# Optimization experiments

Hardware: AMD Instinct MI355X
Metric: run time of the kernel (lower is better)

The kernel has to match this reference:

```python
import jax, jax.numpy as jnp
import numpy as np

NU, NI, E = 20000, 8000, 64
DV, DT = 4096, 768
NE, B = 200000, 4096
L_HET, L_HOMO = 2, 1
K_ISG, K_UCG = 10, 20
MMW, WD = 0.1, 1e-4


def setup_inputs() -> dict:
    ks = jax.random.split(jax.random.key(0), 14)
    return {
        "feat_v": jax.random.normal(ks[0], (NI, DV), jnp.float32),
        "feat_t": jax.random.normal(ks[1], (NI, DT), jnp.float32),
        "pref_v": jax.random.normal(ks[2], (NU, E), jnp.float32) * 0.1,
        "pref_t": jax.random.normal(ks[3], (NU, E), jnp.float32) * 0.1,
        "W_v": jax.random.normal(ks[4], (DV, E), jnp.float32) * 0.02,
        "W_t": jax.random.normal(ks[5], (DT, E), jnp.float32) * 0.02,
        "user_v_alpha": jax.random.normal(ks[6], (1,), jnp.float32),
        "user_nb_weights": jax.random.normal(ks[7], (NU, K_UCG), jnp.float32),
        "edge_users": jax.random.randint(ks[8], (NE,), 0, NU, jnp.int32),
        "edge_items": jax.random.randint(ks[9], (NE,), 0, NI, jnp.int32),
        "u_ids": jax.random.randint(ks[10], (B,), 0, NU, jnp.int32),
        "pos_ids": jax.random.randint(ks[11], (B,), 0, NI, jnp.int32),
        "neg_ids": jax.random.randint(ks[12], (B,), 0, NI, jnp.int32),
        "user_nb": jax.random.randint(ks[13], (NU, K_UCG), 0, NU, jnp.int32),
    }


def reference(feat_v, feat_t, pref_v, pref_t, W_v, W_t, user_v_alpha,
              user_nb_weights, edge_users, edge_items, u_ids, pos_ids,
              neg_ids, user_nb):
    N = NU + NI
    # bidirectional bipartite edges (items offset by NU)
    src = jnp.concatenate([edge_users, edge_items + NU])
    dst = jnp.concatenate([edge_items + NU, edge_users])
    deg = jax.ops.segment_sum(jnp.ones_like(src, jnp.float32), dst, num_segments=N)
    deg = jnp.maximum(deg, 1.0)
    norm = (1.0 / jnp.sqrt(deg[src] * deg[dst]))[:, None]

    def hetero_gcn(feat, pref, W):
        x = jnp.concatenate([pref, feat @ W], axis=0)  # [N, E]
        h, out = x, x
        for _ in range(L_HET):
            h = jax.ops.segment_sum(h[src] * norm, dst, num_segments=N)
            out = out + h
        return out[:NU], out[NU:]

    u_v, i_v = hetero_gcn(feat_v, pref_v, W_v)
    u_t, i_t = hetero_gcn(feat_t, pref_t, W_t)
    a_v = jax.nn.sigmoid(user_v_alpha[0])
    u_f = jnp.concatenate([a_v * u_v, (1.0 - a_v) * u_t], axis=1)  # [NU, 2E]
    i_f = jnp.concatenate([i_v, i_t], axis=1)                      # [NI, 2E]

    # Item Semantic Graph: KNN over cosine sim, no grad through adjacency.
    def knn_adj(f):
        fn = f / jnp.linalg.norm(f, axis=-1, keepdims=True)
        sim = fn @ fn.T                       # [NI, NI]
        _, idx = jax.lax.top_k(sim, K_ISG)
        return jnp.zeros((NI, NI), f.dtype).at[jnp.arange(NI)[:, None], idx].set(1.0)

    adj = jax.lax.stop_gradient(MMW * knn_adj(feat_v) + (1.0 - MMW) * knn_adj(feat_t))
    rs = adj.sum(axis=1)
    adj = adj * jnp.where(rs > 0, 1.0 / rs, 0.0)[:, None]

    h_i = i_f
    for _ in range(L_HOMO):
        h_i = adj @ h_i

    # User Co-occurrence Graph: scatter-softmax attention aggregation, vectorized.
    attn = jax.nn.softmax(user_nb_weights, axis=1)  # [NU, K]
    h_u = u_f
    for _ in range(L_HOMO):
        h_u = jnp.einsum('uk,ukd->ud', attn, h_u[user_nb])

    z_u = u_f + h_u
    z_i = i_f + h_i
    pos = jnp.sum(z_u[u_ids] * z_i[pos_ids], axis=1)
    neg = jnp.sum(z_u[u_ids] * z_i[neg_ids], axis=1)
    bpr = -jnp.mean(jax.nn.log_sigmoid(pos - neg))
    reg = WD * (jnp.sum(pref_v ** 2) + jnp.sum(pref_t ** 2) + user_v_alpha[0] ** 2) / 2.0
    return bpr + reg
```

## Files before the change

kernel.cpp:

```cpp
#include <hip/hip_runtime.h>
#include <cstdint>
#include <cstddef>

#define NU_C   20000
#define NI_C   8000
#define NTOT_C 28000
#define NE_C   200000
#define B_C    4096
#define NPAD_C 8064
#define NCHUNK 63
#define NPAIR  2016

typedef unsigned short u16;
typedef unsigned int   u32;
typedef unsigned char  u8;
typedef __bf16 bf16x8 __attribute__((ext_vector_type(8)));
typedef float  f32x4  __attribute__((ext_vector_type(4)));

static __device__ __forceinline__ u16 f2bf(float f) {
  u32 u = __float_as_uint(f);
  return (u16)((u + 0x7fffu + ((u >> 16) & 1u)) >> 16);
}

static __device__ __forceinline__ void gl_lds16(const void* g, void* l) {
  __builtin_amdgcn_global_load_lds(
      (const __attribute__((address_space(1))) void*)g,
      (__attribute__((address_space(3))) void*)l, 16, 0, 0);
}

static __device__ __forceinline__ int xcd_swz(int b) {
  return (b & 7) * (NPAIR / 8) + (b >> 3);
}

__global__ void conv_kernel2(const float* __restrict__ Fv, const float* __restrict__ Ft,
                             u16* __restrict__ Fbv, u16* __restrict__ Fbt,
                             u8* __restrict__ Fv8,
                             float* __restrict__ rnv, float* __restrict__ rnt) {
  int b = blockIdx.x;
  const int tid = threadIdx.x;
  float ss = 0.f;
  if (b < NPAD_C) {
    const int row = b;
    u16* dst  = Fbv + (size_t)row * 4096;
    u8*  dst8 = Fv8 + (size_t)row * 4096;
    if (row < NI_C) {
      const float* src = Fv + (size_t)row * 4096;
      for (int c = tid * 4; c < 4096; c += 1024) {
        float4 f = *(const float4*)(src + c);
        ss += f.x*f.x + f.y*f.y + f.z*f.z + f.w*f.w;
        ushort4 v; v.x = f2bf(f.x); v.y = f2bf(f.y); v.z = f2bf(f.z); v.w = f2bf(f.w);
        *(ushort4*)(dst + c) = v;
        int w8 = __builtin_amdgcn_cvt_pk_fp8_f32(f.x, f.y, 0, false);
        w8 = __builtin_amdgcn_cvt_pk_fp8_f32(f.z, f.w, w8, true);
        *(u32*)(dst8 + c) = (u32)w8;
      }
    } else {
      for (int c = tid * 4; c < 4096; c += 1024) {
        ushort4 v; v.x = v.y = v.z = v.w = 0;
        *(ushort4*)(dst + c) = v;
        *(u32*)(dst8 + c) = 0u;
      }
    }
    #pragma unroll
    for (int off = 32; off; off >>= 1) ss += __shfl_xor(ss, off);
    __shared__ float red[4];
    if ((tid & 63) == 0) red[tid >> 6] = ss;
    __syncthreads();
    if (tid == 0) {
      float s = red[0] + red[1] + red[2] + red[3];
      rnv[row] = (row < NI_C) ? rsqrtf(s) : 0.f;
    }
  } else {
    const int row = b - NPAD_C;
    u16* dst = Fbt + (size_t)row * 768;
    if (row < NI_C) {
      const float* src = Ft + (size_t)row * 768;
      for (int c = tid * 4; c < 768; c += 1024) {
        float4 f = *(const float4*)(src + c);
        ss += f.x*f.x + f.y*f.y + f.z*f.z + f.w*f.w;
        ushort4 v; v.x = f2bf(f.x); v.y = f2bf(f.y); v.z = f2bf(f.z); v.w = f2bf(f.w);
        *(ushort4*)(dst + c) = v;
      }
    } else {
      for (int c = tid * 4; c < 768; c += 1024) {
        ushort4 v; v.x = v.y = v.z = v.w = 0;
        *(ushort4*)(dst + c) = v;
      }
    }
    #pragma unroll
    for (int off = 32; off; off >>= 1) ss += __shfl_xor(ss, off);
    __shared__ float red[4];
    if ((tid & 63) == 0) red[tid >> 6] = ss;
    __syncthreads();
    if (tid == 0) {
      float s = red[0] + red[1] + red[2] + red[3];
      rnt[row] = (row < NI_C) ? rsqrtf(s) : 0.f;
    }
  }
}

__launch_bounds__(256)
__global__ void simtopk_sym_fp8_kernel(const u8* __restrict__ F, const float* __restrict__ rn,
                                       u32* __restrict__ tv) {
  __shared__ __align__(16) char smem[34816];
  u8*    sB   = (u8*)smem;
  u8*    sA   = (u8*)(smem + 16384);
  float* T    = (float*)smem;
  int*   mk   = (int*)smem;
  int*   mk2  = (int*)(smem + 20480);
  float* sRNI = (float*)(smem + 33792);
  float* sRNJ = (float*)(smem + 34304);

  const int tid  = threadIdx.x;
  const int lane = tid & 63;
  const int wv   = tid >> 6;
  const int n15  = lane & 15;
  const int quad = lane >> 4;

  int I = 0, rem = xcd_swz(blockIdx.x);
  { int rowlen = NCHUNK;
    while (rem >= rowlen) { rem -= rowlen; rowlen--; I++; } }
  const int J = I + rem;

  const int l2   = lane >> 2;
  const int lseg = (lane & 3) ^ (l2 & 3) ^ (lane >> 4);
  const u8* gB[2]; const u8* gA[2]; u8* lB[2]; u8* lA[2];
  #pragma unroll
  for (int rep = 0; rep < 2; ++rep) {
    int row = wv * 32 + rep * 16 + l2;
    gB[rep] = F + (size_t)(I * 128 + row) * 4096 + lseg * 16;
    gA[rep] = F + (size_t)(J * 128 + row) * 4096 + lseg * 16;
    lB[rep] = sB + (wv * 32 + rep * 16) * 64;
    lA[rep] = sA + (wv * 32 + rep * 16) * 64;
  }
  const int s_n = (n15 & 3) ^ (n15 >> 2);
  const int q2  = quad >> 1;
  const int q8  = (quad & 1) * 8;
  const int rB0 = (wv * 32 + n15) * 64;
  const int rB1 = rB0 + 16 * 64;

  f32x4 acc[2][8];
  #pragma unroll
  for (int tf = 0; tf < 2; ++tf)
    #pragma unroll
    for (int af = 0; af < 8; ++af) { f32x4 z = {0.f,0.f,0.f,0.f}; acc[tf][af] = z; }

  for (int k0 = 0; k0 < 4096; k0 += 128) {
    __syncthreads();
    gl_lds16(gB[0] + k0,      lB[0]);
    gl_lds16(gB[0] + k0 + 64, lB[0] + 8192);
    gl_lds16(gB[1] + k0,      lB[1]);
    gl_lds16(gB[1] + k0 + 64, lB[1] + 8192);
    gl_lds16(gA[0] + k0,      lA[0]);
    gl_lds16(gA[0] + k0 + 64, lA[0] + 8192);
    gl_lds16(gA[1] + k0,      lA[1]);
    gl_lds16(gA[1] + k0 + 64, lA[1] + 8192);
    if (k0 == 0) {
      if (tid < 128) sRNJ[tid] = rn[J * 128 + tid];
      else           sRNI[tid - 128] = rn[I * 128 + (tid - 128)];
    }
    __syncthreads();
    #pragma unroll
    for (int ksub = 0; ksub < 2; ++ksub) {
      const u8* bBase = sB + ksub * 8192;
      const u8* aBase = sA + ksub * 8192;
      #pragma unroll
      for (int ks = 0; ks < 2; ++ks) {
        const int sw = (((ks * 2 + q2) ^ s_n) << 4) + q8;
        long long b0 = *(const long long*)(bBase + rB0 + sw);
        long long b1 = *(const long long*)(bBase + rB1 + sw);
        #pragma unroll
        for (int af = 0; af < 8; ++af) {
          long long a = *(const long long*)(aBase + (af * 16 + n15) * 64 + sw);
          acc[0][af] = __builtin_amdgcn_mfma_f32_16x16x32_fp8_fp8(a, b0, acc[0][af], 0, 0, 0);
          acc[1][af] = __builtin_amdgcn_mfma_f32_16x16x32_fp8_fp8(a, b1, acc[1][af], 0, 0, 0);
        }
      }
    }
  }

  int bk[2][10];
  #pragma unroll
  for (int tf = 0; tf < 2; ++tf)
    #pragma unroll
    for (int j = 0; j < 10; ++j) bk[tf][j] = 0;

  #pragma unroll
  for (int af = 0; af < 8; ++af) {
    const float4 rn4 = *(const float4*)(sRNJ + af * 16 + quad * 4);
    const float rna[4] = {rn4.x, rn4.y, rn4.z, rn4.w};
    #pragma unroll
    for (int r = 0; r < 4; ++r) {
      const int ci = J * 128 + af * 16 + quad * 4 + r;
      #pragma unroll
      for (int tf = 0; tf < 2; ++tf) {
        float v = acc[tf][af][r] * rna[r];
        int key = (int)((__float_as_uint(v) & 0xFFFFE000u) | (u32)ci);
        if (ci < NI_C && key > bk[tf][9]) {
          bk[tf][9] = key;
          #pragma unroll
          for (int j = 9; j > 0; --j)
            if (bk[tf][j] > bk[tf][j-1]) { int t = bk[tf][j]; bk[tf][j] = bk[tf][j-1]; bk[tf][j-1] = t; }
        }
      }
    }
  }
  __syncthreads();
  #pragma unroll
  for (int tf = 0; tf < 2; ++tf) {
    int rl = wv * 32 + tf * 16 + n15;
    #pragma unroll
    for (int j = 0; j < 10; ++j) mk[rl * 40 + quad * 10 + j] = bk[tf][j];
  }
  __syncthreads();
  if (tid < 128) {
    int* m = mk + tid * 40;
    int h0 = 0, h1 = 10, h2 = 20, h3 = 30;
    int v0 = m[0], v1 = m[10], v2 = m[20], v3 = m[30];
    #pragma unroll
    for (int s = 0; s < 10; ++s) {
      int m01 = v0 > v1 ? v0 : v1, m23 = v2 > v3 ? v2 : v3;
      int mx = m01 > m23 ? m01 : m23;
      mk2[tid * 10 + s] = mx;
      if      (mx == v0) { ++h0; v0 = (h0 < 10) ? m[h0] : (int)0x80000000; }
      else if (mx == v1) { ++h1; v1 = (h1 < 20) ? m[h1] : (int)0x80000000; }
      else if (mx == v2) { ++h2; v2 = (h2 < 30) ? m[h2] : (int)0x80000000; }
      else               { ++h3; v3 = (h3 < 40) ? m[h3] : (int)0x80000000; }
    }
  }
  __syncthreads();
  { u32* o = tv + ((size_t)J * NPAD_C + I * 128) * 10;
    for (int g = tid; g < 1280; g += 256) o[g] = (u32)mk2[g]; }

  if (I == J) return;

  int bj[2][10];
  #pragma unroll
  for (int s = 0; s < 2; ++s)
    #pragma unroll
    for (int j = 0; j < 10; ++j) bj[s][j] = 0;

  #pragma unroll
  for (int tf = 0; tf < 2; ++tf) {
    __syncthreads();
    #pragma unroll
    for (int af = 0; af < 8; ++af)
      #pragma unroll
      for (int r = 0; r < 4; ++r)
        T[(af * 16 + quad * 4 + r) * 66 + wv * 16 + n15] = acc[tf][af][r];
    __syncthreads();
    #pragma unroll
    for (int s = 0; s < 2; ++s) {
      const int c_own = wv * 32 + s * 16 + n15;
      #pragma unroll
      for (int j = 0; j < 16; ++j) {
        const int t  = quad * 32 + tf * 16 + j;
        const int t64 = quad * 16 + j;
        float v = T[c_own * 66 + t64] * sRNI[t];
        const int ti = I * 128 + t;
        int key = (int)((__float_as_uint(v) & 0xFFFFE000u) | (u32)ti);
        if (ti < NI_C && key > bj[s][9]) {
          bj[s][9] = key;
          #pragma unroll
          for (int q = 9; q > 0; --q)
            if (bj[s][q] > bj[s][q-1]) { int tt = bj[s][q]; bj[s][q] = bj[s][q-1]; bj[s][q-1] = tt; }
        }
      }
    }
  }
  __syncthreads();
  #pragma unroll
  for (int s = 0; s < 2; ++s) {
    int rl = wv * 32 + s * 16 + n15;
    #pragma unroll
    for (int j = 0; j < 10; ++j) mk[rl * 40 + quad * 10 + j] = bj[s][j];
  }
  __syncthreads();
  if (tid < 128) {
    int* m = mk + tid * 40;
    int h0 = 0, h1 = 10, h2 = 20, h3 = 30;
    int v0 = m[0], v1 = m[10], v2 = m[20], v3 = m[30];
    #pragma unroll
    for (int s = 0; s < 10; ++s) {
      int m01 = v0 > v1 ? v0 : v1, m23 = v2 > v3 ? v2 : v3;
      int mx = m01 > m23 ? m01 : m23;
      mk2[tid * 10 + s] = mx;
      if      (mx == v0) { ++h0; v0 = (h0 < 10) ? m[h0] : (int)0x80000000; }
      else if (mx == v1) { ++h1; v1 = (h1 < 20) ? m[h1] : (int)0x80000000; }
      else if (mx == v2) { ++h2; v2 = (h2 < 30) ? m[h2] : (int)0x80000000; }
      else               { ++h3; v3 = (h3 < 40) ? m[h3] : (int)0x80000000; }
    }
  }
  __syncthreads();
  { u32* o = tv + ((size_t)I * NPAD_C + J * 128) * 10;
    for (int g = tid; g < 1280; g += 256) o[g] = (u32)mk2[g]; }
}

template<int D>
__launch_bounds__(256)
__global__ void simtopk_sym_kernel(const u16* __restrict__ F, const float* __restrict__ rn,
                                   u32* __restrict__ tv) {
  __shared__ __align__(16) char smem[40960];
  u16*   sB   = (u16*)smem;
  u16*   sA   = (u16*)(smem + 16384);
  float* T    = (float*)smem;
  int*   mk   = (int*)smem;
  int*   mk2  = (int*)(smem + 20480);
  float* sRNI = (float*)(smem + 34816);
  float* sRNJ = (float*)(smem + 35328);

  const int tid  = threadIdx.x;
  const int lane = tid & 63;
  const int wv   = tid >> 6;
  const int n15  = lane & 15;
  const int quad = lane >> 4;

  int I = 0, rem = xcd_swz(blockIdx.x);
  { int rowlen = NCHUNK;
    while (rem >= rowlen) { rem -= rowlen; rowlen--; I++; } }
  const int J = I + rem;

  const int l8  = lane >> 3;
  const int sgu = ((lane & 7) ^ l8) << 3;
  const u16* gB[4]; const u16* gA[4]; u16* lB[4]; u16* lA[4];
  #pragma unroll
  for (int rep = 0; rep < 4; ++rep) {
    int row = wv * 32 + rep * 8 + l8;
    gB[rep] = F + (size_t)(I * 128 + row) * D + sgu;
    gA[rep] = F + (size_t)(J * 128 + row) * D + sgu;
    lB[rep] = sB + wv * 2048 + rep * 512;
    lA[rep] = sA + wv * 2048 + rep * 512;
  }
  const int swu0 = ((quad    ) ^ (n15 & 7)) << 3;
  const int swu1 = ((quad + 4) ^ (n15 & 7)) << 3;
  const int rowB0 = (wv * 32 + n15) * 64;
  const int rowB1 = rowB0 + 16 * 64;

  f32x4 acc[2][8];
  #pragma unroll
  for (int tf = 0; tf < 2; ++tf)
    #pragma unroll
    for (int af = 0; af < 8; ++af) { f32x4 z = {0.f,0.f,0.f,0.f}; acc[tf][af] = z; }

  for (int k0 = 0; k0 < D; k0 += 64) {
    __syncthreads();
    #pragma unroll
    for (int rep = 0; rep < 4; ++rep) gl_lds16(gB[rep] + k0, lB[rep]);
    #pragma unroll
    for (int rep = 0; rep < 4; ++rep) gl_lds16(gA[rep] + k0, lA[rep]);
    if (k0 == 0) {
      if (tid < 128) sRNJ[tid] = rn[J * 128 + tid];
      else           sRNI[tid - 128] = rn[I * 128 + (tid - 128)];
    }
    __syncthreads();
    #pragma unroll
    for (int ks = 0; ks < 2; ++ks) {
      const int swu = ks ? swu1 : swu0;
      bf16x8 b0 = *(const bf16x8*)(sB + rowB0 + swu);
      bf16x8 b1 = *(const bf16x8*)(sB + rowB1 + swu);
      #pragma unroll
      for (int af = 0; af < 8; ++af) {
        bf16x8 a = *(const bf16x8*)(sA + (af * 16 + n15) * 64 + swu);
        acc[0][af] = __builtin_amdgcn_mfma_f32_16x16x32_bf16(a, b0, acc[0][af], 0, 0, 0);
        acc[1][af] = __builtin_amdgcn_mfma_f32_16x16x32_bf16(a, b1, acc[1][af], 0, 0, 0);
      }
    }
  }

  int bk[2][10];
  #pragma unroll
  for (int tf = 0; tf < 2; ++tf)
    #pragma unroll
    for (int j = 0; j < 10; ++j) bk[tf][j] = 0;

  #pragma unroll
  for (int af = 0; af < 8; ++af) {
    const float4 rn4 = *(const float4*)(sRNJ + af * 16 + quad * 4);
    const float rna[4] = {rn4.x, rn4.y, rn4.z, rn4.w};
    #pragma unroll
    for (int r = 0; r < 4; ++r) {
      const int ci = J * 128 + af * 16 + quad * 4 + r;
      #pragma unroll
      for (int tf = 0; tf < 2; ++tf) {
        float v = acc[tf][af][r] * rna[r];
        int key = (int)((__float_as_uint(v) & 0xFFFFE000u) | (u32)ci);
        if (ci < NI_C && key > bk[tf][9]) {
          bk[tf][9] = key;
          #pragma unroll
          for (int j = 9; j > 0; --j)
            if (bk[tf][j] > bk[tf][j-1]) { int t = bk[tf][j]; bk[tf][j] = bk[tf][j-1]; bk[tf][j-1] = t; }
        }
      }
    }
  }
  __syncthreads();
  #pragma unroll
  for (int tf = 0; tf < 2; ++tf) {
    int rl = wv * 32 + tf * 16 + n15;
    #pragma unroll
    for (int j = 0; j < 10; ++j) mk[rl * 40 + quad * 10 + j] = bk[tf][j];
  }
  __syncthreads();
  if (tid < 128) {
    int* m = mk + tid * 40;
    int h0 = 0, h1 = 10, h2 = 20, h3 = 30;
    int v0 = m[0], v1 = m[10], v2 = m[20], v3 = m[30];
    #pragma unroll
    for (int s = 0; s < 10; ++s) {
      int m01 = v0 > v1 ? v0 : v1, m23 = v2 > v3 ? v2 : v3;
      int mx = m01 > m23 ? m01 : m23;
      mk2[tid * 10 + s] = mx;
      if      (mx == v0) { ++h0; v0 = (h0 < 10) ? m[h0] : (int)0x80000000; }
      else if (mx == v1) { ++h1; v1 = (h1 < 20) ? m[h1] : (int)0x80000000; }
      else if (mx == v2) { ++h2; v2 = (h2 < 30) ? m[h2] : (int)0x80000000; }
      else               { ++h3; v3 = (h3 < 40) ? m[h3] : (int)0x80000000; }
    }
  }
  __syncthreads();
  { u32* o = tv + ((size_t)J * NPAD_C + I * 128) * 10;
    for (int g = tid; g < 1280; g += 256) o[g] = (u32)mk2[g]; }

  if (I == J) return;

  int bj[2][10];
  #pragma unroll
  for (int s = 0; s < 2; ++s)
    #pragma unroll
    for (int j = 0; j < 10; ++j) bj[s][j] = 0;

  #pragma unroll
  for (int tf = 0; tf < 2; ++tf) {
    __syncthreads();
    #pragma unroll
    for (int af = 0; af < 8; ++af)
      #pragma unroll
      for (int r = 0; r < 4; ++r)
        T[(af * 16 + quad * 4 + r) * 66 + wv * 16 + n15] = acc[tf][af][r];
    __syncthreads();
    #pragma unroll
    for (int s = 0; s < 2; ++s) {
      const int c_own = wv * 32 + s * 16 + n15;
      #pragma unroll
      for (int j = 0; j < 16; ++j) {
        const int t  = quad * 32 + tf * 16 + j;
        const int t64 = quad * 16 + j;
        float v = T[c_own * 66 + t64] * sRNI[t];
        const int ti = I * 128 + t;
        int key = (int)((__float_as_uint(v) & 0xFFFFE000u) | (u32)ti);
        if (ti < NI_C && key > bj[s][9]) {
          bj[s][9] = key;
          #pragma unroll
          for (int q = 9; q > 0; --q)
            if (bj[s][q] > bj[s][q-1]) { int tt = bj[s][q]; bj[s][q] = bj[s][q-1]; bj[s][q-1] = tt; }
        }
      }
    }
  }
  __syncthreads();
  #pragma unroll
  for (int s = 0; s < 2; ++s) {
    int rl = wv * 32 + s * 16 + n15;
    #pragma unroll
    for (int j = 0; j < 10; ++j) mk[rl * 40 + quad * 10 + j] = bj[s][j];
  }
  __syncthreads();
  if (tid < 128) {
    int* m = mk + tid * 40;
    int h0 = 0, h1 = 10, h2 = 20, h3 = 30;
    int v0 = m[0], v1 = m[10], v2 = m[20], v3 = m[30];
    #pragma unroll
    for (int s = 0; s < 10; ++s) {
      int m01 = v0 > v1 ? v0 : v1, m23 = v2 > v3 ? v2 : v3;
      int mx = m01 > m23 ? m01 : m23;
      mk2[tid * 10 + s] = mx;
      if      (mx == v0) { ++h0; v0 = (h0 < 10) ? m[h0] : (int)0x80000000; }
      else if (mx == v1) { ++h1; v1 = (h1 < 20) ? m[h1] : (int)0x80000000; }
      else if (mx == v2) { ++h2; v2 = (h2 < 30) ? m[h2] : (int)0x80000000; }
      else               { ++h3; v3 = (h3 < 40) ? m[h3] : (int)0x80000000; }
    }
  }
  __syncthreads();
  { u32* o = tv + ((size_t)I * NPAD_C + J * 128) * 10;
    for (int g = tid; g < 1280; g += 256) o[g] = (u32)mk2[g]; }
}

__global__ void merge_topk_kernel(const u32* __restrict__ tv, int* __restrict__ idx) {
  __shared__ int fk[640];
  const int row = blockIdx.x;
  const int tid = threadIdx.x;
  for (int g = tid; g < 630; g += 64)
    fk[g] = (int)tv[((size_t)(g / 10) * NPAD_C + row) * 10 + (g % 10)];
  if (tid < 10) fk[630 + tid] = (int)0x80000000;
  __syncthreads();
  int v[10];
  #pragma unroll
  for (int j = 0; j < 10; ++j) v[j] = fk[tid + j * 64];
  #pragma unroll 1
  for (int s = 0; s < 10; ++s) {
    int loc = v[0];
    #pragma unroll
    for (int j = 1; j < 10; ++j) loc = v[j] > loc ? v[j] : loc;
    #pragma unroll
    for (int off = 32; off; off >>= 1) {
      int o = __shfl_xor(loc, off); loc = o > loc ? o : loc;
    }
    if (tid == 0) idx[row * 10 + s] = loc & 0x1FFF;
    #pragma unroll
    for (int j = 0; j < 10; ++j) if (v[j] == loc) v[j] = (int)0x80000000;
  }
}

__global__ void deg_count_kernel(const int* __restrict__ eu, const int* __restrict__ ei,
                                 float* deg) {
  int e = blockIdx.x * 256 + threadIdx.x;
  if (e < NE_C) {
    atomicAdd(&deg[eu[e]], 1.f);
    atomicAdd(&deg[NU_C + ei[e]], 1.f);
  }
}

__global__ void scan_kernel(float* __restrict__ deg, int* __restrict__ row_start,
                            int* __restrict__ cursor) {
  __shared__ int part[1024];
  const int tid = threadIdx.x;
  const int base = tid * 28;
  float dl[28];
  int local[28];
  int s = 0;
  #pragma unroll
  for (int j = 0; j < 28; ++j) {
    int n = base + j;
    float df = (n < NTOT_C) ? deg[n] : 0.f;
    dl[j] = df;
    local[j] = s; s += (int)df;
  }
  part[tid] = s;
  __syncthreads();
  for (int off = 1; off < 1024; off <<= 1) {
    int v = (tid >= off) ? part[tid - off] : 0;
    __syncthreads();
    part[tid] += v;
    __syncthreads();
  }
  int pre = (tid > 0) ? part[tid - 1] : 0;
  #pragma unroll
  for (int j = 0; j < 28; ++j) {
    int n = base + j;
    if (n < NTOT_C) {
      row_start[n] = pre + local[j];
      cursor[n]    = pre + local[j];
      deg[n]       = rsqrtf(fmaxf(dl[j], 1.f));
    }
  }
  if (tid == 1023) row_start[NTOT_C] = part[1023];
}

__global__ void place_kernel(const int* __restrict__ eu, const int* __restrict__ ei,
                             const float* __restrict__ dinv, int* __restrict__ cursor,
                             int* __restrict__ esrc, float* __restrict__ ew) {
  int e = blockIdx.x * 256 + threadIdx.x;
  if (e >= NE_C) return;
  int u = eu[e], v = NU_C + ei[e];
  float w = dinv[u] * dinv[v];
  int p1 = atomicAdd(&cursor[v], 1);  esrc[p1] = u; ew[p1] = w;
  int p2 = atomicAdd(&cursor[u], 1);  esrc[p2] = v; ew[p2] = w;
}

__global__ void wtrans_kernel(const float* __restrict__ Wv, const float* __restrict__ Wti,
                              u16* __restrict__ Ov, u16* __restrict__ Ot) {
  __shared__ u16 sT[64][72];
  int b = blockIdx.x;
  const float* W; u16* O; int D;
  if (b < 64) { W = Wv; O = Ov; D = 4096; }
  else        { b -= 64; W = Wti; O = Ot; D = 768; }
  const int k0 = b * 64;
  const int r = threadIdx.x >> 6;
  const int c = threadIdx.x & 63;
  for (int rr = r; rr < 64; rr += 4)
    sT[c][rr] = f2bf(W[(size_t)(k0 + rr) * 64 + c]);
  __syncthreads();
  const int n = threadIdx.x >> 2, seg = threadIdx.x & 3;
  uint4 a0 = *(const uint4*)&sT[n][seg * 16];
  uint4 a1 = *(const uint4*)&sT[n][seg * 16 + 8];
  *(uint4*)(O + (size_t)n * D + k0 + seg * 16)     = a0;
  *(uint4*)(O + (size_t)n * D + k0 + seg * 16 + 8) = a1;
}

template<int D>
__launch_bounds__(256)
__global__ void gemm_xw_kernel(const u16* __restrict__ F, const u16* __restrict__ Wt,
                               float* __restrict__ x2, int modeoff) {
  __shared__ __align__(16) u16 sF[64 * 64];
  const int tid  = threadIdx.x;
  const int lane = tid & 63;
  const int wv   = tid >> 6;
  const int n15  = lane & 15;
  const int quad = lane >> 4;
  const int l8   = lane >> 3;
  const int sgu  = ((lane & 7) ^ l8) << 3;
  const u16* gF[2]; u16* lF[2];
  #pragma unroll
  for (int rep = 0; rep < 2; ++rep) {
    int row = rep * 32 + wv * 8 + l8;
    gF[rep] = F + (size_t)(blockIdx.x * 64 + row) * D + sgu;
    lF[rep] = sF + (rep * 32 + wv * 8) * 64;
  }
  const int swu0 = ((quad    ) ^ (n15 & 7)) << 3;
  const int swu1 = ((quad + 4) ^ (n15 & 7)) << 3;

  f32x4 acc[4];
  #pragma unroll
  for (int nf = 0; nf < 4; ++nf) { f32x4 z = {0.f,0.f,0.f,0.f}; acc[nf] = z; }

  for (int k0 = 0; k0 < D; k0 += 64) {
    __syncthreads();
    gl_lds16(gF[0] + k0, lF[0]);
    gl_lds16(gF[1] + k0, lF[1]);
    __syncthreads();
    #pragma unroll
    for (int ks = 0; ks < 2; ++ks) {
      const int swu = ks ? swu1 : swu0;
      bf16x8 a = *(const bf16x8*)(sF + (wv * 16 + n15) * 64 + swu);
      #pragma unroll
      for (int nf = 0; nf < 4; ++nf) {
        bf16x8 b = *(const bf16x8*)(Wt + (size_t)(nf * 16 + n15) * D + k0 + ks * 32 + quad * 8);
        acc[nf] = __builtin_amdgcn_mfma_f32_16x16x32_bf16(a, b, acc[nf], 0, 0, 0);
      }
    }
  }
  #pragma unroll
  for (int nf = 0; nf < 4; ++nf)
    #pragma unroll
    for (int r = 0; r < 4; ++r) {
      int row = blockIdx.x * 64 + wv * 16 + quad * 4 + r;
      if (row < NI_C)
        x2[(size_t)(NU_C + row) * 128 + modeoff + nf * 16 + n15] = acc[nf][r];
    }
}

__global__ void fill_pref_kernel(const float* __restrict__ pv, const float* __restrict__ pt,
                                 float* __restrict__ x2) {
  int gid = blockIdx.x * 256 + threadIdx.x;
  int u = gid >> 7, c = gid & 127;
  x2[gid] = (c < 64) ? pv[(size_t)u * 64 + c] : pt[(size_t)u * 64 + (c - 64)];
}

__global__ void gather2_kernel(const int* __restrict__ row_start, const int* __restrict__ esrc,
                               const float* __restrict__ ew, const float* __restrict__ x2,
                               float* __restrict__ h1) {
  const int node = blockIdx.x * 2 + (threadIdx.x >> 7);
  const int ch   = threadIdx.x & 127;
  if (node >= NTOT_C) return;
  const int b = row_start[node], e = row_start[node + 1];
  float acc = 0.f;
  for (int i = b; i < e; ++i)
    acc += ew[i] * x2[(size_t)esrc[i] * 128 + ch];
  h1[(size_t)node * 128 + ch] = acc;
}

__global__ void gather_comb2_kernel(const int* __restrict__ row_start, const int* __restrict__ esrc,
                                    const float* __restrict__ ew, const float* __restrict__ x2,
                                    const float* __restrict__ h1, const float* __restrict__ alpha,
                                    float* __restrict__ uf, float* __restrict__ ifb) {
  const int node = blockIdx.x * 2 + (threadIdx.x >> 7);
  const int ch   = threadIdx.x & 127;
  if (node >= NTOT_C) return;
  const int b = row_start[node], e = row_start[node + 1];
  float acc = 0.f;
  for (int i = b; i < e; ++i)
    acc += ew[i] * h1[(size_t)esrc[i] * 128 + ch];
  float val = x2[(size_t)node * 128 + ch] + h1[(size_t)node * 128 + ch] + acc;
  if (node < NU_C) {
    float av = 1.f / (1.f + expf(-alpha[0]));
    float coef = (ch < 64) ? av : (1.f - av);
    uf[(size_t)node * 128 + ch] = coef * val;
  } else {
    ifb[(size_t)(node - NU_C) * 128 + ch] = val;
  }
}

__global__ void zuzi_kernel(const float* __restrict__ uf, const float* __restrict__ w,
                            const int* __restrict__ nb, const float* __restrict__ ifb,
                            const int* __restrict__ iv, const int* __restrict__ it,
                            float* __restrict__ zu, float* __restrict__ zi) {
  const int c = threadIdx.x;
  if (blockIdx.x < NU_C) {
    const int u = blockIdx.x;
    __shared__ float at[20];
    if (c < 20) at[c] = w[u * 20 + c];
    __syncthreads();
    float e[20]; float m = -1e30f;
    #pragma unroll
    for (int k = 0; k < 20; ++k) { e[k] = at[k]; m = fmaxf(m, e[k]); }
    float ssum = 0.f;
    #pragma unroll
    for (int k = 0; k < 20; ++k) { e[k] = expf(e[k] - m); ssum += e[k]; }
    float inv = 1.f / ssum;
    float acc = 0.f;
    #pragma unroll
    for (int k = 0; k < 20; ++k) {
      int j = nb[u * 20 + k];
      acc += e[k] * inv * uf[(size_t)j * 128 + c];
    }
    zu[(size_t)u * 128 + c] = uf[(size_t)u * 128 + c] + acc;
  } else {
    const int i = blockIdx.x - NU_C;
    float sv = 0.f, st = 0.f;
    #pragma unroll
    for (int k = 0; k < 10; ++k) sv += ifb[(size_t)iv[i * 10 + k] * 128 + c];
    #pragma unroll
    for (int k = 0; k < 10; ++k) st += ifb[(size_t)it[i * 10 + k] * 128 + c];
    zi[(size_t)i * 128 + c] = ifb[(size_t)i * 128 + c] + 0.01f * sv + 0.09f * st;
  }
}

__global__ void loss_kernel(const float* __restrict__ zu, const float* __restrict__ zi,
                            const int* __restrict__ uid, const int* __restrict__ pid,
                            const int* __restrict__ nid, const float* __restrict__ pv,
                            const float* __restrict__ pt, const float* __restrict__ alpha,
                            float* __restrict__ out) {
  if (blockIdx.x < 1024) {
    int wv = threadIdx.x >> 6, lane = threadIdx.x & 63;
    int b = blockIdx.x * 4 + wv;
    int u = uid[b], p = pid[b], n = nid[b];
    float2 a  = *(const float2*)(zu + (size_t)u * 128 + lane * 2);
    float2 xp = *(const float2*)(zi + (size_t)p * 128 + lane * 2);
    float2 xn = *(const float2*)(zi + (size_t)n * 128 + lane * 2);
    float d = a.x * (xp.x - xn.x) + a.y * (xp.y - xn.y);
    #pragma unroll
    for (int off = 32; off; off >>= 1) d += __shfl_xor(d, off);
    if (lane == 0) {
      float xv = -d;
      float sp = fmaxf(xv, 0.f) + log1pf(expf(-fabsf(xv)));
      atomicAdd(out, sp * (1.f / (float)B_C));
    }
  } else {
    const size_t N1 = (size_t)NU_C * 64;
    float acc = 0.f;
    for (size_t i = (size_t)(blockIdx.x - 1024) * 256 + threadIdx.x; i < 2 * N1;
         i += (size_t)512 * 256) {
      float x = (i < N1) ? pv[i] : pt[i - N1];
      acc += x * x;
    }
    #pragma unroll
    for (int off = 32; off; off >>= 1) acc += __shfl_xor(acc, off);
    __shared__ float red[4];
    if ((threadIdx.x & 63) == 0) red[threadIdx.x >> 6] = acc;
    __syncthreads();
    if (threadIdx.x == 0) {
      float s = red[0] + red[1] + red[2] + red[3];
      atomicAdd(out, 0.5e-4f * s);
    }
    if (blockIdx.x == 1024 && threadIdx.x == 0) {
      float a = alpha[0];
      atomicAdd(out, 0.5e-4f * a * a);
    }
  }
}

extern "C" void kernel_launch(void* const* d_in, const int* in_sizes, int n_in,
                              void* d_out, int out_size, void* d_ws, size_t ws_size,
                              hipStream_t stream) {
  const float* feat_v = (const float*)d_in[0];
  const float* feat_t = (const float*)d_in[1];
  const float* pref_v = (const float*)d_in[2];
  const float* pref_t = (const float*)d_in[3];
  const float* W_v    = (const float*)d_in[4];
  const float* W_t    = (const float*)d_in[5];
  const float* alpha  = (const float*)d_in[6];
  const float* unw    = (const float*)d_in[7];
  const int* eu       = (const int*)d_in[8];
  const int* ei       = (const int*)d_in[9];
  const int* u_ids    = (const int*)d_in[10];
  const int* pos_ids  = (const int*)d_in[11];
  const int* neg_ids  = (const int*)d_in[12];
  const int* user_nb  = (const int*)d_in[13];
  float* out = (float*)d_out;
  char* ws = (char*)d_ws;

  size_t off = 0;
  auto alloc = [&](size_t bytes) { char* p = ws + off; off += (bytes + 255) & ~(size_t)255; return p; };
  u16*   fvbf  = (u16*)alloc((size_t)NPAD_C * 4096 * 2);
  u8*    fv8   = (u8*)alloc((size_t)NPAD_C * 4096);
  u16*   ftbf  = (u16*)alloc((size_t)NPAD_C * 768 * 2);
  u16*   wtv   = (u16*)alloc((size_t)64 * 4096 * 2);
  u16*   wtt   = (u16*)alloc((size_t)64 * 768 * 2);
  float* rn_v  = (float*)alloc(NPAD_C * 4);
  float* rn_t  = (float*)alloc(NPAD_C * 4);
  int*   idx_v = (int*)alloc(NI_C * 10 * 4);
  int*   idx_t = (int*)alloc(NI_C * 10 * 4);
  float* dinv  = (float*)alloc(NTOT_C * 4);
  int*   rowst = (int*)alloc((NTOT_C + 1) * 4);
  int*   curs  = (int*)alloc(NTOT_C * 4);
  int*   esrc  = (int*)alloc((size_t)2 * NE_C * 4);
  float* ew    = (float*)alloc((size_t)2 * NE_C * 4);
  float* x2    = (float*)alloc((size_t)NTOT_C * 128 * 4);
  float* h1    = (float*)alloc((size_t)NTOT_C * 128 * 4);
  char*  pC    = alloc((size_t)(NU_C + NI_C) * 128 * 4 * 2);
  u32*   tvb   = (u32*)pC;
  float* u_f   = (float*)pC;
  float* i_f   = (float*)(pC + (size_t)NU_C * 128 * 4);
  float* z_u   = (float*)(pC + (size_t)(NU_C + NI_C) * 128 * 4);
  float* z_i   = (float*)(pC + (size_t)(2 * NU_C + NI_C) * 128 * 4);

  hipMemsetAsync(out, 0, sizeof(float), stream);
  hipMemsetAsync(dinv, 0, NTOT_C * 4, stream);

  deg_count_kernel<<<(NE_C + 255) / 256, 256, 0, stream>>>(eu, ei, dinv);
  scan_kernel<<<1, 1024, 0, stream>>>(dinv, rowst, curs);
  place_kernel<<<(NE_C + 255) / 256, 256, 0, stream>>>(eu, ei, dinv, curs, esrc, ew);

  conv_kernel2<<<2 * NPAD_C, 256, 0, stream>>>(feat_v, feat_t, fvbf, ftbf, fv8, rn_v, rn_t);
  wtrans_kernel<<<76, 256, 0, stream>>>(W_v, W_t, wtv, wtt);

  simtopk_sym_fp8_kernel<<<NPAIR, 256, 0, stream>>>(fv8, rn_v, tvb);
  merge_topk_kernel<<<NI_C, 64, 0, stream>>>(tvb, idx_v);
  simtopk_sym_kernel<768><<<NPAIR, 256, 0, stream>>>(ftbf, rn_t, tvb);
  merge_topk_kernel<<<NI_C, 64, 0, stream>>>(tvb, idx_t);

  fill_pref_kernel<<<(NU_C * 128) / 256, 256, 0, stream>>>(pref_v, pref_t, x2);
  gemm_xw_kernel<4096><<<125, 256, 0, stream>>>(fvbf, wtv, x2, 0);
  gemm_xw_kernel<768><<<125, 256, 0, stream>>>(ftbf, wtt, x2, 64);
  gather2_kernel<<<14000, 256, 0, stream>>>(rowst, esrc, ew, x2, h1);
  gather_comb2_kernel<<<14000, 256, 0, stream>>>(rowst, esrc, ew, x2, h1, alpha, u_f, i_f);

  zuzi_kernel<<<NU_C + NI_C, 128, 0, stream>>>(u_f, unw, user_nb, i_f, idx_v, idx_t, z_u, z_i);
  loss_kernel<<<1536, 256, 0, stream>>>(z_u, z_i, u_ids, pos_ids, neg_ids,
                                        pref_v, pref_t, alpha, out);
}
```

Baseline: 1.085 ms.

## Fuse independent stages into multi-role kernels to overlap topk, GEMM and gathers

Merges independent work into combined launches: the fp8 similarity top-k runs alongside the feature-projection GEMMs and the pref fill, the first gather runs with the visual top-k merge, and the text top-k runs with the second gather. Each block dispatches on its block index. The merge kernel now processes four rows per 256-thread block instead of one row per 64-thread block. The text top-k partials go to a second scratch buffer that aliases the bf16 visual features, which are no longer needed once the first fused kernel finishes. This cuts launch count and tail idle time, at the cost of heterogeneous blocks sharing one LDS size and register budget, which can lower occupancy for the lighter roles.

```diff
diff --git a/kernel.cpp b/kernel.cpp
--- a/kernel.cpp
+++ b/kernel.cpp
@@ -99,10 +99,9 @@
   }
 }
 
-__launch_bounds__(256)
-__global__ void simtopk_sym_fp8_kernel(const u8* __restrict__ F, const float* __restrict__ rn,
-                                       u32* __restrict__ tv) {
-  __shared__ __align__(16) char smem[34816];
+static __device__ __forceinline__ void simtopk_fp8_body(
+    int bid, char* smem, const u8* __restrict__ F, const float* __restrict__ rn,
+    u32* __restrict__ tv) {
   u8*    sB   = (u8*)smem;
   u8*    sA   = (u8*)(smem + 16384);
   float* T    = (float*)smem;
@@ -117,7 +116,7 @@
   const int n15  = lane & 15;
   const int quad = lane >> 4;
 
-  int I = 0, rem = xcd_swz(blockIdx.x);
+  int I = 0, rem = xcd_swz(bid);
   { int rowlen = NCHUNK;
     while (rem >= rowlen) { rem -= rowlen; rowlen--; I++; } }
   const int J = I + rem;
@@ -296,11 +295,9 @@
     for (int g = tid; g < 1280; g += 256) o[g] = (u32)mk2[g]; }
 }
 
-template<int D>
-__launch_bounds__(256)
-__global__ void simtopk_sym_kernel(const u16* __restrict__ F, const float* __restrict__ rn,
-                                   u32* __restrict__ tv) {
-  __shared__ __align__(16) char smem[40960];
+static __device__ __forceinline__ void simtopk_bf16_body(
+    int bid, char* smem, const u16* __restrict__ F, const float* __restrict__ rn,
+    u32* __restrict__ tv) {
   u16*   sB   = (u16*)smem;
   u16*   sA   = (u16*)(smem + 16384);
   float* T    = (float*)smem;
@@ -315,7 +312,7 @@
   const int n15  = lane & 15;
   const int quad = lane >> 4;
 
-  int I = 0, rem = xcd_swz(blockIdx.x);
+  int I = 0, rem = xcd_swz(bid);
   { int rowlen = NCHUNK;
     while (rem >= rowlen) { rem -= rowlen; rowlen--; I++; } }
   const int J = I + rem;
@@ -326,8 +323,8 @@
   #pragma unroll
   for (int rep = 0; rep < 4; ++rep) {
     int row = wv * 32 + rep * 8 + l8;
-    gB[rep] = F + (size_t)(I * 128 + row) * D + sgu;
-    gA[rep] = F + (size_t)(J * 128 + row) * D + sgu;
+    gB[rep] = F + (size_t)(I * 128 + row) * 768 + sgu;
+    gA[rep] = F + (size_t)(J * 128 + row) * 768 + sgu;
     lB[rep] = sB + wv * 2048 + rep * 512;
     lA[rep] = sA + wv * 2048 + rep * 512;
   }
@@ -342,7 +339,7 @@
     #pragma unroll
     for (int af = 0; af < 8; ++af) { f32x4 z = {0.f,0.f,0.f,0.f}; acc[tf][af] = z; }
 
-  for (int k0 = 0; k0 < D; k0 += 64) {
+  for (int k0 = 0; k0 < 768; k0 += 64) {
     __syncthreads();
     #pragma unroll
     for (int rep = 0; rep < 4; ++rep) gl_lds16(gB[rep] + k0, lB[rep]);
@@ -484,17 +481,20 @@
     for (int g = tid; g < 1280; g += 256) o[g] = (u32)mk2[g]; }
 }
 
-__global__ void merge_topk_kernel(const u32* __restrict__ tv, int* __restrict__ idx) {
-  __shared__ int fk[640];
-  const int row = blockIdx.x;
-  const int tid = threadIdx.x;
-  for (int g = tid; g < 630; g += 64)
+static __device__ __forceinline__ void merge4_body(int mb, int* fkbase,
+                                                   const u32* __restrict__ tv,
+                                                   int* __restrict__ idx) {
+  const int w    = threadIdx.x >> 6;
+  const int lane = threadIdx.x & 63;
+  const int row  = mb * 4 + w;
+  int* fk = fkbase + w * 640;
+  for (int g = lane; g < 630; g += 64)
     fk[g] = (int)tv[((size_t)(g / 10) * NPAD_C + row) * 10 + (g % 10)];
-  if (tid < 10) fk[630 + tid] = (int)0x80000000;
+  if (lane < 10) fk[630 + lane] = (int)0x80000000;
   __syncthreads();
   int v[10];
   #pragma unroll
-  for (int j = 0; j < 10; ++j) v[j] = fk[tid + j * 64];
+  for (int j = 0; j < 10; ++j) v[j] = fk[lane + j * 64];
   #pragma unroll 1
   for (int s = 0; s < 10; ++s) {
     int loc = v[0];
@@ -504,93 +504,23 @@
     for (int off = 32; off; off >>= 1) {
       int o = __shfl_xor(loc, off); loc = o > loc ? o : loc;
     }
-    if (tid == 0) idx[row * 10 + s] = loc & 0x1FFF;
+    if (lane == 0) idx[row * 10 + s] = loc & 0x1FFF;
     #pragma unroll
     for (int j = 0; j < 10; ++j) if (v[j] == loc) v[j] = (int)0x80000000;
   }
 }
 
-__global__ void deg_count_kernel(const int* __restrict__ eu, const int* __restrict__ ei,
-                                 float* deg) {
-  int e = blockIdx.x * 256 + threadIdx.x;
-  if (e < NE_C) {
-    atomicAdd(&deg[eu[e]], 1.f);
-    atomicAdd(&deg[NU_C + ei[e]], 1.f);
-  }
-}
-
-__global__ void scan_kernel(float* __restrict__ deg, int* __restrict__ row_start,
-                            int* __restrict__ cursor) {
-  __shared__ int part[1024];
-  const int tid = threadIdx.x;
-  const int base = tid * 28;
-  float dl[28];
-  int local[28];
-  int s = 0;
-  #pragma unroll
-  for (int j = 0; j < 28; ++j) {
-    int n = base + j;
-    float df = (n < NTOT_C) ? deg[n] : 0.f;
-    dl[j] = df;
-    local[j] = s; s += (int)df;
-  }
-  part[tid] = s;
-  __syncthreads();
-  for (int off = 1; off < 1024; off <<= 1) {
-    int v = (tid >= off) ? part[tid - off] : 0;
-    __syncthreads();
-    part[tid] += v;
-    __syncthreads();
-  }
-  int pre = (tid > 0) ? part[tid - 1] : 0;
-  #pragma unroll
-  for (int j = 0; j < 28; ++j) {
-    int n = base + j;
-    if (n < NTOT_C) {
-      row_start[n] = pre + local[j];
-      cursor[n]    = pre + local[j];
-      deg[n]       = rsqrtf(fmaxf(dl[j], 1.f));
-    }
-  }
-  if (tid == 1023) row_start[NTOT_C] = part[1023];
-}
-
-__global__ void place_kernel(const int* __restrict__ eu, const int* __restrict__ ei,
-                             const float* __restrict__ dinv, int* __restrict__ cursor,
-                             int* __restrict__ esrc, float* __restrict__ ew) {
-  int e = blockIdx.x * 256 + threadIdx.x;
-  if (e >= NE_C) return;
-  int u = eu[e], v = NU_C + ei[e];
-  float w = dinv[u] * dinv[v];
-  int p1 = atomicAdd(&cursor[v], 1);  esrc[p1] = u; ew[p1] = w;
-  int p2 = atomicAdd(&cursor[u], 1);  esrc[p2] = v; ew[p2] = w;
-}
-
-__global__ void wtrans_kernel(const float* __restrict__ Wv, const float* __restrict__ Wti,
-                              u16* __restrict__ Ov, u16* __restrict__ Ot) {
-  __shared__ u16 sT[64][72];
-  int b = blockIdx.x;
-  const float* W; u16* O; int D;
-  if (b < 64) { W = Wv; O = Ov; D = 4096; }
-  else        { b -= 64; W = Wti; O = Ot; D = 768; }
-  const int k0 = b * 64;
-  const int r = threadIdx.x >> 6;
-  const int c = threadIdx.x & 63;
-  for (int rr = r; rr < 64; rr += 4)
-    sT[c][rr] = f2bf(W[(size_t)(k0 + rr) * 64 + c]);
-  __syncthreads();
-  const int n = threadIdx.x >> 2, seg = threadIdx.x & 3;
-  uint4 a0 = *(const uint4*)&sT[n][seg * 16];
-  uint4 a1 = *(const uint4*)&sT[n][seg * 16 + 8];
-  *(uint4*)(O + (size_t)n * D + k0 + seg * 16)     = a0;
-  *(uint4*)(O + (size_t)n * D + k0 + seg * 16 + 8) = a1;
+__launch_bounds__(256)
+__global__ void merge4_kernel(const u32* __restrict__ tv, int* __restrict__ idx) {
+  __shared__ int fk[4 * 640];
+  merge4_body(blockIdx.x, fk, tv, idx);
 }
 
 template<int D>
-__launch_bounds__(256)
-__global__ void gemm_xw_kernel(const u16* __restrict__ F, const u16* __restrict__ Wt,
-                               float* __restrict__ x2, int modeoff) {
-  __shared__ __align__(16) u16 sF[64 * 64];
+static __device__ __forceinline__ void gemm_xw_body(
+    int bid, char* smem, const u16* __restrict__ F, const u16* __restrict__ Wt,
+    float* __restrict__ x2, int modeoff) {
+  u16* sF = (u16*)smem;
   const int tid  = threadIdx.x;
   const int lane = tid & 63;
   const int wv   = tid >> 6;
@@ -602,7 +532,7 @@
   #pragma unroll
   for (int rep = 0; rep < 2; ++rep) {
     int row = rep * 32 + wv * 8 + l8;
-    gF[rep] = F + (size_t)(blockIdx.x * 64 + row) * D + sgu;
+    gF[rep] = F + (size_t)(bid * 64 + row) * D + sgu;
     lF[rep] = sF + (rep * 32 + wv * 8) * 64;
   }
   const int swu0 = ((quad    ) ^ (n15 & 7)) << 3;
@@ -632,23 +562,16 @@
   for (int nf = 0; nf < 4; ++nf)
     #pragma unroll
     for (int r = 0; r < 4; ++r) {
-      int row = blockIdx.x * 64 + wv * 16 + quad * 4 + r;
+      int row = bid * 64 + wv * 16 + quad * 4 + r;
       if (row < NI_C)
         x2[(size_t)(NU_C + row) * 128 + modeoff + nf * 16 + n15] = acc[nf][r];
     }
 }
 
-__global__ void fill_pref_kernel(const float* __restrict__ pv, const float* __restrict__ pt,
-                                 float* __restrict__ x2) {
-  int gid = blockIdx.x * 256 + threadIdx.x;
-  int u = gid >> 7, c = gid & 127;
-  x2[gid] = (c < 64) ? pv[(size_t)u * 64 + c] : pt[(size_t)u * 64 + (c - 64)];
-}
-
-__global__ void gather2_kernel(const int* __restrict__ row_start, const int* __restrict__ esrc,
-                               const float* __restrict__ ew, const float* __restrict__ x2,
-                               float* __restrict__ h1) {
-  const int node = blockIdx.x * 2 + (threadIdx.x >> 7);
+static __device__ __forceinline__ void gather2_body(
+    int bid, const int* __restrict__ row_start, const int* __restrict__ esrc,
+    const float* __restrict__ ew, const float* __restrict__ x2, float* __restrict__ h1) {
+  const int node = bid * 2 + (threadIdx.x >> 7);
   const int ch   = threadIdx.x & 127;
   if (node >= NTOT_C) return;
   const int b = row_start[node], e = row_start[node + 1];
@@ -658,11 +581,12 @@
   h1[(size_t)node * 128 + ch] = acc;
 }
 
-__global__ void gather_comb2_kernel(const int* __restrict__ row_start, const int* __restrict__ esrc,
-                                    const float* __restrict__ ew, const float* __restrict__ x2,
-                                    const float* __restrict__ h1, const float* __restrict__ alpha,
-                                    float* __restrict__ uf, float* __restrict__ ifb) {
-  const int node = blockIdx.x * 2 + (threadIdx.x >> 7);
+static __device__ __forceinline__ void gather_comb2_body(
+    int bid, const int* __restrict__ row_start, const int* __restrict__ esrc,
+    const float* __restrict__ ew, const float* __restrict__ x2,
+    const float* __restrict__ h1, const float* __restrict__ alpha,
+    float* __restrict__ uf, float* __restrict__ ifb) {
+  const int node = bid * 2 + (threadIdx.x >> 7);
   const int ch   = threadIdx.x & 127;
   if (node >= NTOT_C) return;
   const int b = row_start[node], e = row_start[node + 1];
@@ -677,6 +601,128 @@
   } else {
     ifb[(size_t)(node - NU_C) * 128 + ch] = val;
   }
+}
+
+__launch_bounds__(256)
+__global__ void fusedA_kernel(const u8* __restrict__ F8, const float* __restrict__ rnv,
+                              u32* __restrict__ tv,
+                              const u16* __restrict__ Fvb, const u16* __restrict__ Wtv,
+                              const u16* __restrict__ Ftb, const u16* __restrict__ Wtt,
+                              float* __restrict__ x2,
+                              const float* __restrict__ pv, const float* __restrict__ pt) {
+  __shared__ __align__(16) char smem[34816];
+  int b = blockIdx.x;
+  if (b < NPAIR) { simtopk_fp8_body(b, smem, F8, rnv, tv); return; }
+  b -= NPAIR;
+  if (b < 125) { gemm_xw_body<4096>(b, smem, Fvb, Wtv, x2, 0); return; }
+  b -= 125;
+  if (b < 125) { gemm_xw_body<768>(b, smem, Ftb, Wtt, x2, 64); return; }
+  b -= 125;
+  {
+    int gid = b * 256 + threadIdx.x;
+    int u = gid >> 7, c = gid & 127;
+    x2[gid] = (c < 64) ? pv[(size_t)u * 64 + c] : pt[(size_t)u * 64 + (c - 64)];
+  }
+}
+
+__launch_bounds__(256)
+__global__ void fusedB_kernel(const int* __restrict__ row_start, const int* __restrict__ esrc,
+                              const float* __restrict__ ew, const float* __restrict__ x2,
+                              float* __restrict__ h1,
+                              const u32* __restrict__ tv, int* __restrict__ idx) {
+  __shared__ int fk[4 * 640];
+  int b = blockIdx.x;
+  if (b < 14000) { gather2_body(b, row_start, esrc, ew, x2, h1); return; }
+  merge4_body(b - 14000, fk, tv, idx);
+}
+
+__launch_bounds__(256)
+__global__ void fusedC_kernel(const u16* __restrict__ Ftb, const float* __restrict__ rnt,
+                              u32* __restrict__ tv2,
+                              const int* __restrict__ row_start, const int* __restrict__ esrc,
+                              const float* __restrict__ ew, const float* __restrict__ x2,
+                              const float* __restrict__ h1, const float* __restrict__ alpha,
+                              float* __restrict__ uf, float* __restrict__ ifb) {
+  __shared__ __align__(16) char smem[40960];
+  int b = blockIdx.x;
+  if (b < NPAIR) { simtopk_bf16_body(b, smem, Ftb, rnt, tv2); return; }
+  gather_comb2_body(b - NPAIR, row_start, esrc, ew, x2, h1, alpha, uf, ifb);
+}
+
+__global__ void deg_count_kernel(const int* __restrict__ eu, const int* __restrict__ ei,
+                                 float* deg) {
+  int e = blockIdx.x * 256 + threadIdx.x;
+  if (e < NE_C) {
+    atomicAdd(&deg[eu[e]], 1.f);
+    atomicAdd(&deg[NU_C + ei[e]], 1.f);
+  }
+}
+
+__global__ void scan_kernel(float* __restrict__ deg, int* __restrict__ row_start,
+                            int* __restrict__ cursor) {
+  __shared__ int part[1024];
+  const int tid = threadIdx.x;
+  const int base = tid * 28;
+  float dl[28];
+  int local[28];
+  int s = 0;
+  #pragma unroll
+  for (int j = 0; j < 28; ++j) {
+    int n = base + j;
+    float df = (n < NTOT_C) ? deg[n] : 0.f;
+    dl[j] = df;
+    local[j] = s; s += (int)df;
+  }
+  part[tid] = s;
+  __syncthreads();
+  for (int off = 1; off < 1024; off <<= 1) {
+    int v = (tid >= off) ? part[tid - off] : 0;
+    __syncthreads();
+    part[tid] += v;
+    __syncthreads();
+  }
+  int pre = (tid > 0) ? part[tid - 1] : 0;
+  #pragma unroll
+  for (int j = 0; j < 28; ++j) {
+    int n = base + j;
+    if (n < NTOT_C) {
+      row_start[n] = pre + local[j];
+      cursor[n]    = pre + local[j];
+      deg[n]       = rsqrtf(fmaxf(dl[j], 1.f));
+    }
+  }
+  if (tid == 1023) row_start[NTOT_C] = part[1023];
+}
+
+__global__ void place_kernel(const int* __restrict__ eu, const int* __restrict__ ei,
+                             const float* __restrict__ dinv, int* __restrict__ cursor,
+                             int* __restrict__ esrc, float* __restrict__ ew) {
+  int e = blockIdx.x * 256 + threadIdx.x;
+  if (e >= NE_C) return;
+  int u = eu[e], v = NU_C + ei[e];
+  float w = dinv[u] * dinv[v];
+  int p1 = atomicAdd(&cursor[v], 1);  esrc[p1] = u; ew[p1] = w;
+  int p2 = atomicAdd(&cursor[u], 1);  esrc[p2] = v; ew[p2] = w;
+}
+
+__global__ void wtrans_kernel(const float* __restrict__ Wv, const float* __restrict__ Wti,
+                              u16* __restrict__ Ov, u16* __restrict__ Ot) {
+  __shared__ u16 sT[64][72];
+  int b = blockIdx.x;
+  const float* W; u16* O; int D;
+  if (b < 64) { W = Wv; O = Ov; D = 4096; }
+  else        { b -= 64; W = Wti; O = Ot; D = 768; }
+  const int k0 = b * 64;
+  const int r = threadIdx.x >> 6;
+  const int c = threadIdx.x & 63;
+  for (int rr = r; rr < 64; rr += 4)
+    sT[c][rr] = f2bf(W[(size_t)(k0 + rr) * 64 + c]);
+  __syncthreads();
+  const int n = threadIdx.x >> 2, seg = threadIdx.x & 3;
+  uint4 a0 = *(const uint4*)&sT[n][seg * 16];
+  uint4 a1 = *(const uint4*)&sT[n][seg * 16 + 8];
+  *(uint4*)(O + (size_t)n * D + k0 + seg * 16)     = a0;
+  *(uint4*)(O + (size_t)n * D + k0 + seg * 16 + 8) = a1;
 }
 
 __global__ void zuzi_kernel(const float* __restrict__ uf, const float* __restrict__ w,
@@ -798,6 +844,7 @@
   float* h1    = (float*)alloc((size_t)NTOT_C * 128 * 4);
   char*  pC    = alloc((size_t)(NU_C + NI_C) * 128 * 4 * 2);
   u32*   tvb   = (u32*)pC;
+  u32*   tvb2  = (u32*)fvbf;
   float* u_f   = (float*)pC;
   float* i_f   = (float*)(pC + (size_t)NU_C * 128 * 4);
   float* z_u   = (float*)(pC + (size_t)(NU_C + NI_C) * 128 * 4);
@@ -809,21 +856,18 @@
   deg_count_kernel<<<(NE_C + 255) / 256, 256, 0, stream>>>(eu, ei, dinv);
   scan_kernel<<<1, 1024, 0, stream>>>(dinv, rowst, curs);
   place_kernel<<<(NE_C + 255) / 256, 256, 0, stream>>>(eu, ei, dinv, curs, esrc, ew);
-
   conv_kernel2<<<2 * NPAD_C, 256, 0, stream>>>(feat_v, feat_t, fvbf, ftbf, fv8, rn_v, rn_t);
   wtrans_kernel<<<76, 256, 0, stream>>>(W_v, W_t, wtv, wtt);
 
-  simtopk_sym_fp8_kernel<<<NPAIR, 256, 0, stream>>>(fv8, rn_v, tvb);
-  merge_topk_kernel<<<NI_C, 64, 0, stream>>>(tvb, idx_v);
-  simtopk_sym_kernel<768><<<NPAIR, 256, 0, stream>>>(ftbf, rn_t, tvb);
-  merge_topk_kernel<<<NI_C, 64, 0, stream>>>(tvb, idx_t);
-
-  fill_pref_kernel<<<(NU_C * 128) / 256, 256, 0, stream>>>(pref_v, pref_t, x2);
-  gemm_xw_kernel<4096><<<125, 256, 0, stream>>>(fvbf, wtv, x2, 0);
-  gemm_xw_kernel<768><<<125, 256, 0, stream>>>(ftbf, wtt, x2, 64);
-  gather2_kernel<<<14000, 256, 0, stream>>>(rowst, esrc, ew, x2, h1);
-  gather_comb2_kernel<<<14000, 256, 0, stream>>>(rowst, esrc, ew, x2, h1, alpha, u_f, i_f);
-
+  fusedA_kernel<<<NPAIR + 250 + 10000, 256, 0, stream>>>(
+      fv8, rn_v, tvb, fvbf, wtv, ftbf, wtt, x2, pref_v, pref_t);
+
+  fusedB_kernel<<<14000 + 2000, 256, 0, stream>>>(rowst, esrc, ew, x2, h1, tvb, idx_v);
+
+  fusedC_kernel<<<NPAIR + 14000, 256, 0, stream>>>(
+      ftbf, rn_t, tvb2, rowst, esrc, ew, x2, h1, alpha, u_f, i_f);
+
+  merge4_kernel<<<2000, 256, 0, stream>>>(tvb2, idx_t);
   zuzi_kernel<<<NU_C + NI_C, 128, 0, stream>>>(u_f, unw, user_nb, i_f, idx_v, idx_t, z_u, z_i);
   loss_kernel<<<1536, 256, 0, stream>>>(z_u, z_i, u_ids, pos_ids, neg_ids,
                                         pref_v, pref_t, alpha, out);
```

After: 1.095 ms. About the same (+0.9%).
